# Kernel tuning notes

Measured on AMD Instinct MI355X. Metric: run time of the kernel, lower is better.

Reference implementation:

```python
import jax, jax.numpy as jnp
import numpy as np

D_CUT = 5.0   # cosine-cutoff distance
SIZE = 128    # rbf size == hidden_channels (nn_dist size = in_channels)
L = 2         # num_layers
EPS = 0.0     # GIN eps (non-trainable, initial 0)


def _rbf(d):
    # d: (E,) distances -> (E, SIZE) expnorm RBF with cosine cutoff
    d = d[:, None]
    start = float(np.exp(-D_CUT))
    means = jnp.linspace(start, 1.0, SIZE)
    beta = (2.0 / SIZE * (1.0 - start)) ** (-2)
    dc = jnp.minimum(d, D_CUT)
    cutoff = 0.5 * (jnp.cos(dc * jnp.pi / D_CUT) + 1.0)
    return cutoff * jnp.exp(-beta * (jnp.exp(-d) - means) ** 2)


def setup_inputs() -> dict:
    key = jax.random.key(0)
    ks = jax.random.split(key, 40)
    it = iter(range(40))
    def k():
        return ks[next(it)]
    N, H, ED, AS = 100000, 128, 4, 4
    def w(shape, s):
        return jax.random.normal(k(), shape, jnp.float32) * s
    inp = {}
    inp['x_lig'] = jax.random.normal(k(), (N, H), jnp.float32)
    inp['x_pock'] = jax.random.normal(k(), (N, H), jnp.float32)
    for name, E in (('bond', 200000), ('lp', 400000), ('pl', 400000)):
        inp['ei_' + name] = jax.random.randint(k(), (2, E), 0, N, jnp.int32)
        inp['ew_' + name] = jax.random.uniform(k(), (E,), jnp.float32) * D_CUT
        inp['ea_' + name] = jax.random.normal(k(), (E, AS), jnp.float32)
    inp['W0'] = w((3, AS, ED), 0.5)                 # initial per-edge-type lins (no bias)
    inp['Wd'] = w((L, 3, H, 2 * H), H ** -0.5)      # RBFDistanceScaleShift lin
    inp['bd'] = jnp.zeros((L, 3, 2 * H), jnp.float32)
    inp['We'] = w((L, 3, ED, H), 0.5)               # EGINConv.lin (edge_dim -> hidden)
    inp['be'] = jnp.zeros((L, 3, H), jnp.float32)
    inp['W1'] = w((L, 3, H, H), H ** -0.5)          # nn_node MLP layer 1
    inp['b1'] = jnp.zeros((L, 3, H), jnp.float32)
    inp['W2'] = w((L, 3, H, H), H ** -0.5)          # nn_node MLP layer 2
    inp['b2'] = jnp.zeros((L, 3, H), jnp.float32)
    return inp


def reference(x_lig, x_pock, ei_bond, ew_bond, ea_bond, ei_lp, ew_lp, ea_lp,
              ei_pl, ew_pl, ea_pl, W0, Wd, bd, We, be, W1, b1, W2, b2):
    # HeteroEGIN.forward: initial per-edge-type linear on raw edge attrs (bias-free)
    ea0 = ea_bond @ W0[0]
    ea1 = ea_lp @ W0[1]
    ea2 = ea_pl @ W0[2]

    def conv(x_src, x_dst, ei, ew, ea, t, l):
        # EGINConv per edge type t, layer l
        ss = _rbf(ew) @ Wd[l, t] + bd[l, t]            # (E, 2H) scale/shift from distance
        scale, shift = jnp.split(ss, 2, axis=1)
        xj = x_src[ei[0]] + (ea @ We[l, t] + be[l, t])  # gather + edge-attr lin
        msg = jax.nn.relu(xj * scale + shift)           # gated message
        agg = jax.ops.segment_sum(msg, ei[1], num_segments=x_dst.shape[0])
        o = agg + (1.0 + EPS) * x_dst
        return jax.nn.relu(o @ W1[l, t] + b1[l, t]) @ W2[l, t] + b2[l, t]

    for l in range(L):
        # to_hetero: sum conv outputs across edge types per destination node type
        new_lig = (conv(x_lig, x_lig, ei_bond, ew_bond, ea0, 0, l)
                   + conv(x_pock, x_lig, ei_pl, ew_pl, ea2, 2, l))
        new_pock = conv(x_lig, x_pock, ei_lp, ew_lp, ea1, 1, l)
        if l < L - 1:  # BasicGNN: act between layers, none after last (jk=None)
            new_lig = jax.nn.relu(new_lig)
            new_pock = jax.nn.relu(new_pock)
        x_lig, x_pock = new_lig, new_pock
    return jnp.concatenate([x_lig, x_pock], axis=0)
```

## Files before the change

kernel.cpp:

```cpp
#include <hip/hip_runtime.h>
#include <hip/hip_bf16.h>
#include <hip/hip_fp16.h>
#include <cmath>

typedef __attribute__((ext_vector_type(8))) short short8_t;
typedef __attribute__((ext_vector_type(4))) float f32x4;

static __device__ __forceinline__ short f2bs(float f) {
    union { __hip_bfloat16 h; short s; } u;
    u.h = __float2bfloat16(f);
    return u.s;
}
static __device__ __forceinline__ float bs2f(unsigned int us) {
    union { float f; unsigned int i; } u;
    u.i = us << 16;
    return u.f;
}
static __device__ __forceinline__ unsigned int pack2bf(float a, float b) {
    return (unsigned int)(unsigned short)f2bs(a) |
           ((unsigned int)(unsigned short)f2bs(b) << 16);
}
static __device__ __forceinline__ void lds_barrier() {
    asm volatile("s_waitcnt lgkmcnt(0)\n\ts_barrier" ::: "memory");
}

__global__ void pack_kernel(const float* __restrict__ Wd,
                            const float* __restrict__ W1,
                            const float* __restrict__ W2,
                            const float* __restrict__ W0,
                            const float* __restrict__ We,
                            short* __restrict__ pWd,
                            short* __restrict__ pW1,
                            short* __restrict__ pW2,
                            float* __restrict__ Mb)
{
    const int tid = blockIdx.x * blockDim.x + threadIdx.x;
    const int stride = gridDim.x * blockDim.x;
    for (int i = tid; i < 6 * 32768; i += stride) {
        int c = i >> 15, rem = i & 32767;
        int f = rem >> 9, l = (rem >> 3) & 63, j = rem & 7;
        int kk = f >> 4, nt = f & 15;
        int k = kk * 32 + (l >> 4) * 8 + j;
        int n = nt * 16 + (l & 15);
        pWd[i] = f2bs(Wd[(size_t)c * 32768 + k * 256 + n]);
    }
    for (int i = tid; i < 6 * 16384; i += stride) {
        int c = i >> 14, rem = i & 16383;
        int f = rem >> 9, l = (rem >> 3) & 63, j = rem & 7;
        int kk = f >> 3, nt = f & 7;
        int k = kk * 32 + (l >> 4) * 8 + j;
        int n = nt * 16 + (l & 15);
        pW1[i] = f2bs(W1[(size_t)c * 16384 + k * 128 + n]);
        pW2[i] = f2bs(W2[(size_t)c * 16384 + k * 128 + n]);
    }
    for (int i = tid; i < 6 * 512; i += stride) {
        int c = i >> 9, rem = i & 511;
        int a = rem >> 7, h = rem & 127;
        int t = c % 3;
        float m = 0.f;
        #pragma unroll
        for (int j = 0; j < 4; ++j)
            m = fmaf(W0[t * 16 + a * 4 + j], We[(size_t)c * 512 + j * 128 + h], m);
        Mb[i] = m;
    }
}

__global__ void tobf16_kernel(const float* __restrict__ a, const float* __restrict__ b,
                              unsigned short* __restrict__ oa, unsigned short* __restrict__ ob,
                              int n4)
{
    int i = blockIdx.x * blockDim.x + threadIdx.x;
    const int stride = gridDim.x * blockDim.x;
    for (; i < n4; i += stride) {
        float4 va = ((const float4*)a)[i];
        uint2 pa; pa.x = pack2bf(va.x, va.y); pa.y = pack2bf(va.z, va.w);
        ((uint2*)oa)[i] = pa;
        float4 vb = ((const float4*)b)[i];
        uint2 pb; pb.x = pack2bf(vb.x, vb.y); pb.y = pack2bf(vb.z, vb.w);
        ((uint2*)ob)[i] = pb;
    }
}

__global__ void hist3_kernel(const int* __restrict__ eiB, const int* __restrict__ eiL,
                             const int* __restrict__ eiP,
                             int EB, int EL, int EP, int N, int* __restrict__ cnt3)
{
    const int total = EB + EL + EP;
    for (int e = blockIdx.x * blockDim.x + threadIdx.x; e < total;
         e += gridDim.x * blockDim.x) {
        int base, le; const int* ei; int E;
        if (e < EB)           { base = 0;     le = e;           ei = eiB; E = EB; }
        else if (e < EB + EL) { base = N;     le = e - EB;      ei = eiL; E = EL; }
        else                  { base = 2 * N; le = e - EB - EL; ei = eiP; E = EP; }
        atomicAdd(&cnt3[base + ei[E + le]], 1);
    }
}

__global__ void scan1k_kernel(int* __restrict__ data, int* __restrict__ bsum, int n)
{
    __shared__ int buf[1024];
    const int gid = blockIdx.x * 1024 + threadIdx.x;
    int v = (gid < n) ? data[gid] : 0;
    buf[threadIdx.x] = v;
    __syncthreads();
    for (int off = 1; off < 1024; off <<= 1) {
        int t = (threadIdx.x >= off) ? buf[threadIdx.x - off] : 0;
        __syncthreads();
        buf[threadIdx.x] += t;
        __syncthreads();
    }
    if (gid < n) data[gid] = buf[threadIdx.x] - v;
    if (bsum && threadIdx.x == 1023) bsum[blockIdx.x] = buf[1023];
}

__global__ void scan_add_kernel(int* __restrict__ data, const int* __restrict__ bsum,
                                int* __restrict__ cursor, int n)
{
    const int gid = blockIdx.x * 1024 + threadIdx.x;
    if (gid < n) {
        int v = data[gid] + bsum[blockIdx.x];
        data[gid] = v;
        cursor[gid] = v;
    }
}

__global__ void scatter3_kernel(const int* __restrict__ eiB, const float* __restrict__ ewB,
                                const float4* __restrict__ eaB,
                                const int* __restrict__ eiL, const float* __restrict__ ewL,
                                const float4* __restrict__ eaL,
                                const int* __restrict__ eiP, const float* __restrict__ ewP,
                                const float4* __restrict__ eaP,
                                int EB, int EL, int EP, int N,
                                int* __restrict__ cursor,
                                uint4* __restrict__ rec, float* __restrict__ ewp)
{
    const int total = EB + EL + EP;
    for (int e = blockIdx.x * blockDim.x + threadIdx.x; e < total;
         e += gridDim.x * blockDim.x) {
        int base, le; const int* ei; const float* ew; const float4* ea; int E;
        if (e < EB)           { base = 0;     le = e;           ei = eiB; ew = ewB; ea = eaB; E = EB; }
        else if (e < EB + EL) { base = N;     le = e - EB;      ei = eiL; ew = ewL; ea = eaL; E = EL; }
        else                  { base = 2 * N; le = e - EB - EL; ei = eiP; ew = ewP; ea = eaP; E = EP; }
        int d = ei[E + le];
        int p = atomicAdd(&cursor[base + d], 1);
        float4 a = ea[le];
        uint4 r;
        r.x = (unsigned int)ei[le];
        r.y = (unsigned int)d;
        r.z = pack2bf(a.x, a.y);
        r.w = pack2bf(a.z, a.w);
        rec[p] = r;
        ewp[p] = ew[le];
    }
}

__global__ __launch_bounds__(512, 2)
void edge_mfma_kernel(
    const unsigned short* __restrict__ xsb,
    const uint4* __restrict__ rec,
    const float* __restrict__ ewp,
    const short* __restrict__ pWd, const float* __restrict__ bd,
    const float* __restrict__ Mb, const float* __restrict__ be,
    float* __restrict__ agg,
    int E, int ntiles,
    float rs, float rstep, float rbeta)
{
    __shared__ short sRbf[64 * 128];
    __shared__ __half sSS[64 * 256];

    const int t = threadIdx.x;
    const int lane = t & 63;
    const int w = t >> 6;
    const int l15 = lane & 15;
    const int l4 = lane >> 4;

    short8_t bfrag[4][2];
    #pragma unroll
    for (int kk = 0; kk < 4; ++kk)
        #pragma unroll
        for (int i = 0; i < 2; ++i)
            bfrag[kk][i] = *(const short8_t*)&pWd[((kk * 16 + 2 * w + i) * 64 + lane) * 8];
    float bdv[2];
    #pragma unroll
    for (int i = 0; i < 2; ++i) bdv[i] = bd[(2 * w + i) * 16 + l15];
    const float be0 = be[2 * lane], be1 = be[2 * lane + 1];
    float ma0[4], ma1[4];
    #pragma unroll
    for (int a = 0; a < 4; ++a) {
        ma0[a] = Mb[a * 128 + 2 * lane];
        ma1[a] = Mb[a * 128 + 2 * lane + 1];
    }

    const int stride = gridDim.x;
    int tile = blockIdx.x;
    if (tile >= ntiles) return;

    float ew_c; int src_c, dst_c; unsigned int ea01_c, ea23_c;
    unsigned int gx[8];
    {
        int eL = (tile << 6) + lane;
        int ec = eL < E ? eL : E - 1;
        uint4 r = rec[ec];
        ew_c = ewp[ec];
        src_c = (int)r.x;
        dst_c = (eL < E) ? (int)r.y : -1;
        ea01_c = r.z; ea23_c = r.w;
        #pragma unroll
        for (int rr = 0; rr < 8; ++rr) {
            int srn = __shfl(src_c, 8 * w + rr);
            gx[rr] = *(const unsigned int*)&xsb[(size_t)srn * 128 + lane * 2];
        }
    }

    for (; tile < ntiles; tile += stride) {
        const float edv = __expf(-ew_c);
        const float dcc = fminf(ew_c, 5.0f);
        const float cutv = 0.5f * (__cosf(dcc * 0.62831853071795864769f) + 1.0f);
        {
            char* base = (char*)sRbf + lane * 256;
            #pragma unroll
            for (int c = 0; c < 2; ++c) {
                short8_t v;
                #pragma unroll
                for (int j = 0; j < 8; ++j) {
                    float mean = rs + (float)(w * 16 + c * 8 + j) * rstep;
                    float diff = edv - mean;
                    v[j] = f2bs(cutv * __expf(-rbeta * diff * diff));
                }
                *(short8_t*)(base + ((w * 32 + c * 16) ^ ((lane & 7) << 4))) = v;
            }
        }
        unsigned int xjr[8];
        #pragma unroll
        for (int r = 0; r < 8; ++r) {
            unsigned int a01 = __shfl(ea01_c, 8 * w + r);
            unsigned int a23 = __shfl(ea23_c, 8 * w + r);
            float ea0 = bs2f(a01 & 0xffffu), ea1 = bs2f(a01 >> 16);
            float ea2 = bs2f(a23 & 0xffffu), ea3 = bs2f(a23 >> 16);
            unsigned int g = gx[r];
            float x0 = bs2f(g & 0xffffu), x1 = bs2f(g >> 16);
            float o0 = x0 + be0 + ea0 * ma0[0] + ea1 * ma0[1] + ea2 * ma0[2] + ea3 * ma0[3];
            float o1 = x1 + be1 + ea0 * ma1[0] + ea1 * ma1[1] + ea2 * ma1[2] + ea3 * ma1[3];
            xjr[r] = pack2bf(o0, o1);
        }

        lds_barrier();

        const int ntile = tile + stride;
        const bool has_next = ntile < ntiles;
        float ew_n = 0.f; int src_n = 0, dst_n = -1;
        unsigned int ea01_n = 0, ea23_n = 0;
        if (has_next) {
            int eL = (ntile << 6) + lane;
            int ec = eL < E ? eL : E - 1;
            uint4 r = rec[ec];
            ew_n = ewp[ec];
            src_n = (int)r.x;
            dst_n = (eL < E) ? (int)r.y : -1;
            ea01_n = r.z; ea23_n = r.w;
        }
        __builtin_amdgcn_sched_barrier(0);

        f32x4 acc[4][2];
        #pragma unroll
        for (int m = 0; m < 4; ++m) {
            acc[m][0] = (f32x4){0.f, 0.f, 0.f, 0.f};
            acc[m][1] = (f32x4){0.f, 0.f, 0.f, 0.f};
        }
        #pragma unroll
        for (int kk = 0; kk < 4; ++kk) {
            short8_t af[4];
            #pragma unroll
            for (int m = 0; m < 4; ++m) {
                int row = m * 16 + l15;
                int byte = row * 256 + ((kk * 64 + l4 * 16) ^ ((row & 7) << 4));
                af[m] = *(const short8_t*)((const char*)sRbf + byte);
            }
            #pragma unroll
            for (int m = 0; m < 4; ++m)
                #pragma unroll
                for (int i = 0; i < 2; ++i)
                    acc[m][i] = __builtin_amdgcn_mfma_f32_16x16x32_bf16(
                        af[m], bfrag[kk][i], acc[m][i], 0, 0, 0);
        }

        #pragma unroll
        for (int m = 0; m < 4; ++m)
            #pragma unroll
            for (int i = 0; i < 2; ++i) {
                int col = (2 * w + i) * 16 + l15;
                #pragma unroll
                for (int r = 0; r < 4; ++r) {
                    int row = m * 16 + l4 * 4 + r;
                    int byte = row * 512 + ((col * 2) ^ ((row & 7) << 4));
                    *(__half*)((char*)sSS + byte) = __float2half(acc[m][i][r] + bdv[i]);
                }
            }

        if (has_next) {
            #pragma unroll
            for (int r = 0; r < 8; ++r) {
                int srn = __shfl(src_n, 8 * w + r);
                gx[r] = *(const unsigned int*)&xsb[(size_t)srn * 128 + lane * 2];
            }
        }
        const int dst_f = dst_c;
        ew_c = ew_n; src_c = src_n; dst_c = dst_n; ea01_c = ea01_n; ea23_c = ea23_n;

        lds_barrier();

        {
            const bool prev_known = (w > 0);
            const bool next_known = (w < 7);
            const int dst_prev = prev_known ? __shfl(dst_f, 8 * w - 1) : -1;
            const int dst_next = next_known ? __shfl(dst_f, 8 * w + 8) : -1;

            float a0 = 0.f, a1 = 0.f;
            int rdst = __shfl(dst_f, 8 * w);
            bool first_run = true;
            #pragma unroll
            for (int r = 0; r < 8; ++r) {
                int e = 8 * w + r;
                unsigned int sc = *(const unsigned int*)
                    ((const char*)sSS + e * 512 + ((lane * 4) ^ ((e & 7) << 4)));
                unsigned int sh = *(const unsigned int*)
                    ((const char*)sSS + e * 512 + ((256 + lane * 4) ^ ((e & 7) << 4)));
                float2 scf = __half22float2(*(const __half2*)&sc);
                float2 shf = __half22float2(*(const __half2*)&sh);
                unsigned int g = xjr[r];
                float x0 = bs2f(g & 0xffffu), x1 = bs2f(g >> 16);
                float m0 = fmaxf(fmaf(x0, scf.x, shf.x), 0.0f);
                float m1 = fmaxf(fmaf(x1, scf.y, shf.y), 0.0f);
                int d = __shfl(dst_f, e);
                if (d != rdst) {
                    if (rdst >= 0) {
                        bool unsafe = first_run && (!prev_known || dst_prev == rdst);
                        float* ap = &agg[(size_t)rdst * 128 + 2 * lane];
                        if (unsafe) {
                            if (a0 != 0.f) unsafeAtomicAdd(ap, a0);
                            if (a1 != 0.f) unsafeAtomicAdd(ap + 1, a1);
                        } else {
                            float2 v; v.x = a0; v.y = a1;
                            *(float2*)ap = v;
                        }
                    }
                    first_run = false;
                    a0 = 0.f; a1 = 0.f; rdst = d;
                }
                a0 += m0; a1 += m1;
            }
            if (rdst >= 0) {
                bool unsafeL = first_run && (!prev_known || dst_prev == rdst);
                bool unsafeR = (!next_known || dst_next == rdst);
                float* ap = &agg[(size_t)rdst * 128 + 2 * lane];
                if (unsafeL || unsafeR) {
                    if (a0 != 0.f) unsafeAtomicAdd(ap, a0);
                    if (a1 != 0.f) unsafeAtomicAdd(ap + 1, a1);
                } else {
                    float2 v; v.x = a0; v.y = a1;
                    *(float2*)ap = v;
                }
            }
        }
    }
}

__global__ __launch_bounds__(256)
void node_mfma_kernel(
    float* __restrict__ agg,
    const float* __restrict__ xdf, const unsigned short* __restrict__ xdb,
    const short* __restrict__ pW1, const float* __restrict__ b1,
    const short* __restrict__ pW2, const float* __restrict__ b2,
    float* __restrict__ outf, unsigned short* __restrict__ outb,
    int N, int ntiles, int accumulate, int relu_out)
{
    __shared__ short sA[64 * 128];
    __shared__ short sH[64 * 128];

    const int t = threadIdx.x;
    const int lane = t & 63;
    const int w = t >> 6;
    const int l15 = lane & 15;
    const int l4 = lane >> 4;

    short8_t w1f[4][2], w2f[4][2];
    #pragma unroll
    for (int kk = 0; kk < 4; ++kk)
        #pragma unroll
        for (int p = 0; p < 2; ++p) {
            int nt = 2 * w + p;
            w1f[kk][p] = *(const short8_t*)&pW1[((kk * 8 + nt) * 64 + lane) * 8];
            w2f[kk][p] = *(const short8_t*)&pW2[((kk * 8 + nt) * 64 + lane) * 8];
        }
    float b1v[2], b2v[2];
    #pragma unroll
    for (int p = 0; p < 2; ++p) {
        int col = (2 * w + p) * 16 + l15;
        b1v[p] = b1[col];
        b2v[p] = b2[col];
    }

    const float4 zero4 = {0.f, 0.f, 0.f, 0.f};

    for (int tile = blockIdx.x; tile < ntiles; tile += gridDim.x) {
        const int n0 = tile << 6;
        #pragma unroll
        for (int i = 0; i < 4; ++i) {
            int idx = i * 256 + t;
            int row = idx >> 4, c8 = idx & 15;
            int gr = n0 + row; if (gr >= N) gr = N - 1;
            float4 a0 = ((const float4*)agg)[(size_t)gr * 32 + c8 * 2];
            float4 a1 = ((const float4*)agg)[(size_t)gr * 32 + c8 * 2 + 1];
            ((float4*)agg)[(size_t)gr * 32 + c8 * 2]     = zero4;
            ((float4*)agg)[(size_t)gr * 32 + c8 * 2 + 1] = zero4;
            float av[8] = {a0.x, a0.y, a0.z, a0.w, a1.x, a1.y, a1.z, a1.w};
            float xv[8];
            if (xdf) {
                float4 x0 = ((const float4*)xdf)[(size_t)gr * 32 + c8 * 2];
                float4 x1 = ((const float4*)xdf)[(size_t)gr * 32 + c8 * 2 + 1];
                xv[0] = x0.x; xv[1] = x0.y; xv[2] = x0.z; xv[3] = x0.w;
                xv[4] = x1.x; xv[5] = x1.y; xv[6] = x1.z; xv[7] = x1.w;
            } else {
                uint4 xr = ((const uint4*)xdb)[(size_t)gr * 16 + c8];
                xv[0] = bs2f(xr.x & 0xffffu); xv[1] = bs2f(xr.x >> 16);
                xv[2] = bs2f(xr.y & 0xffffu); xv[3] = bs2f(xr.y >> 16);
                xv[4] = bs2f(xr.z & 0xffffu); xv[5] = bs2f(xr.z >> 16);
                xv[6] = bs2f(xr.w & 0xffffu); xv[7] = bs2f(xr.w >> 16);
            }
            short8_t v;
            #pragma unroll
            for (int j = 0; j < 8; ++j)
                v[j] = f2bs(av[j] + xv[j]);
            int byte = row * 256 + ((c8 * 16) ^ ((row & 7) << 4));
            *(short8_t*)((char*)sA + byte) = v;
        }
        lds_barrier();

        f32x4 acc[4][2];
        #pragma unroll
        for (int m = 0; m < 4; ++m) {
            acc[m][0] = (f32x4){0.f, 0.f, 0.f, 0.f};
            acc[m][1] = (f32x4){0.f, 0.f, 0.f, 0.f};
        }
        #pragma unroll
        for (int kk = 0; kk < 4; ++kk) {
            short8_t af[4];
            #pragma unroll
            for (int m = 0; m < 4; ++m) {
                int row = m * 16 + l15;
                int byte = row * 256 + ((kk * 64 + l4 * 16) ^ ((row & 7) << 4));
                af[m] = *(const short8_t*)((const char*)sA + byte);
            }
            #pragma unroll
            for (int m = 0; m < 4; ++m)
                #pragma unroll
                for (int p = 0; p < 2; ++p)
                    acc[m][p] = __builtin_amdgcn_mfma_f32_16x16x32_bf16(
                        af[m], w1f[kk][p], acc[m][p], 0, 0, 0);
        }
        #pragma unroll
        for (int m = 0; m < 4; ++m)
            #pragma unroll
            for (int p = 0; p < 2; ++p) {
                int col = (2 * w + p) * 16 + l15;
                #pragma unroll
                for (int r = 0; r < 4; ++r) {
                    int row = m * 16 + l4 * 4 + r;
                    short hs = f2bs(fmaxf(acc[m][p][r] + b1v[p], 0.f));
                    int byte = row * 256 + ((col * 2) ^ ((row & 7) << 4));
                    *(short*)((char*)sH + byte) = hs;
                }
            }
        lds_barrier();

        f32x4 acc2[4][2];
        #pragma unroll
        for (int m = 0; m < 4; ++m) {
            acc2[m][0] = (f32x4){0.f, 0.f, 0.f, 0.f};
            acc2[m][1] = (f32x4){0.f, 0.f, 0.f, 0.f};
        }
        #pragma unroll
        for (int kk = 0; kk < 4; ++kk) {
            short8_t af[4];
            #pragma unroll
            for (int m = 0; m < 4; ++m) {
                int row = m * 16 + l15;
                int byte = row * 256 + ((kk * 64 + l4 * 16) ^ ((row & 7) << 4));
                af[m] = *(const short8_t*)((const char*)sH + byte);
            }
            #pragma unroll
            for (int m = 0; m < 4; ++m)
                #pragma unroll
                for (int p = 0; p < 2; ++p)
                    acc2[m][p] = __builtin_amdgcn_mfma_f32_16x16x32_bf16(
                        af[m], w2f[kk][p], acc2[m][p], 0, 0, 0);
        }
        #pragma unroll
        for (int m = 0; m < 4; ++m)
            #pragma unroll
            for (int p = 0; p < 2; ++p) {
                int col = (2 * w + p) * 16 + l15;
                #pragma unroll
                for (int r = 0; r < 4; ++r) {
                    int row = n0 + m * 16 + l4 * 4 + r;
                    if (row < N) {
                        float v = acc2[m][p][r] + b2v[p];
                        if (outf) {
                            float* op = &outf[(size_t)row * 128 + col];
                            if (accumulate) v += *op;
                            if (relu_out) v = fmaxf(v, 0.f);
                            *op = v;
                        } else {
                            unsigned short* op = &outb[(size_t)row * 128 + col];
                            if (accumulate) v += bs2f((unsigned int)*op);
                            if (relu_out) v = fmaxf(v, 0.f);
                            *op = (unsigned short)f2bs(v);
                        }
                    }
                }
            }
    }
}

extern "C" void kernel_launch(void* const* d_in, const int* in_sizes, int n_in,
                              void* d_out, int out_size, void* d_ws, size_t ws_size,
                              hipStream_t stream)
{
    const float* x_lig   = (const float*)d_in[0];
    const float* x_pock  = (const float*)d_in[1];
    const int*   ei_bond = (const int*)d_in[2];
    const float* ew_bond = (const float*)d_in[3];
    const float* ea_bond = (const float*)d_in[4];
    const int*   ei_lp   = (const int*)d_in[5];
    const float* ew_lp   = (const float*)d_in[6];
    const float* ea_lp   = (const float*)d_in[7];
    const int*   ei_pl   = (const int*)d_in[8];
    const float* ew_pl   = (const float*)d_in[9];
    const float* ea_pl   = (const float*)d_in[10];
    const float* W0 = (const float*)d_in[11];
    const float* Wd = (const float*)d_in[12];
    const float* bd = (const float*)d_in[13];
    const float* We = (const float*)d_in[14];
    const float* be = (const float*)d_in[15];
    const float* W1 = (const float*)d_in[16];
    const float* b1 = (const float*)d_in[17];
    const float* W2 = (const float*)d_in[18];
    const float* b2 = (const float*)d_in[19];

    const int H = 128;
    const int N = in_sizes[0] / H;
    const int E_bond = in_sizes[3];
    const int E_lp   = in_sizes[6];
    const int E_pl   = in_sizes[9];
    const int E_all  = E_bond + E_lp + E_pl;

    char* wp = (char*)d_ws;
    auto alloc = [&](size_t bytes) -> char* {
        char* r = wp;
        wp += (bytes + 255) & ~(size_t)255;
        return r;
    };
    unsigned short* A   = (unsigned short*)alloc((size_t)N * H * 2);
    unsigned short* Bb  = (unsigned short*)alloc((size_t)N * H * 2);
    unsigned short* C   = (unsigned short*)alloc((size_t)N * H * 2);
    float*   agg  = (float*)alloc((size_t)N * H * 4);
    int*     cnt3 = (int*)alloc((size_t)3 * N * 4);
    char*    zero_end = wp;
    uint4*   recAll = (uint4*)alloc((size_t)E_all * 16);
    float*   ewpAll = (float*)alloc((size_t)E_all * 4);
    short*   pWd  = (short*)alloc(6 * 32768 * 2);
    short*   pW1s = (short*)alloc(6 * 16384 * 2);
    short*   pW2s = (short*)alloc(6 * 16384 * 2);
    float*   Mb   = (float*)alloc(6 * 512 * 4);
    int*     cursor = (int*)alloc((size_t)3 * N * 4);
    int*     bsum   = (int*)alloc(1024 * 4);

    const uint4* recB = recAll;
    const uint4* recL = recAll + E_bond;
    const uint4* recP = recAll + E_bond + E_lp;
    const float* ewpB = ewpAll;
    const float* ewpL = ewpAll + E_bond;
    const float* ewpP = ewpAll + E_bond + E_lp;

    float* outL = (float*)d_out;
    float* outP = outL + (size_t)N * H;

    const int capE = 256;
    const int capN = 4 * 256;

    hipMemsetAsync(agg, 0, (size_t)(zero_end - (char*)agg), stream);
    tobf16_kernel<<<512, 256, 0, stream>>>(x_lig, x_pock, A, Bb, N * H / 4);
    pack_kernel<<<256, 256, 0, stream>>>(Wd, W1, W2, W0, We, pWd, pW1s, pW2s, Mb);

    const int n3 = 3 * N;
    const int nb3 = (n3 + 1023) / 1024;
    hist3_kernel<<<1024, 256, 0, stream>>>(ei_bond, ei_lp, ei_pl,
                                           E_bond, E_lp, E_pl, N, cnt3);
    scan1k_kernel<<<nb3, 1024, 0, stream>>>(cnt3, bsum, n3);
    scan1k_kernel<<<1, 1024, 0, stream>>>(bsum, nullptr, nb3);
    scan_add_kernel<<<nb3, 1024, 0, stream>>>(cnt3, bsum, cursor, n3);
    scatter3_kernel<<<1024, 256, 0, stream>>>(
        ei_bond, ew_bond, (const float4*)ea_bond,
        ei_lp,   ew_lp,   (const float4*)ea_lp,
        ei_pl,   ew_pl,   (const float4*)ea_pl,
        E_bond, E_lp, E_pl, N, cursor, recAll, ewpAll);

    const double start_d = exp(-5.0);
    const float rs    = (float)start_d;
    const float rstep = (float)((1.0 - start_d) / 127.0);
    const float rbeta = (float)std::pow(2.0 / 128.0 * (1.0 - start_d), -2.0);

    auto conv = [&](const unsigned short* src,
                    const float* xdf, const unsigned short* xdb,
                    const uint4* rec, const float* ewp, int E,
                    int l, int tt, float* outf, unsigned short* outb,
                    int accum, int relu) {
        const int lt = l * 3 + tt;
        const int ntE = (E + 63) / 64;
        const int gE = ntE < capE ? ntE : capE;
        edge_mfma_kernel<<<gE, 512, 0, stream>>>(
            src, rec, ewp,
            pWd + (size_t)lt * 32768, bd + (size_t)lt * 256,
            Mb + (size_t)lt * 512, be + (size_t)lt * 128,
            agg, E, ntE, rs, rstep, rbeta);
        const int ntN = (N + 63) / 64;
        const int gN = ntN < capN ? ntN : capN;
        node_mfma_kernel<<<gN, 256, 0, stream>>>(
            agg, xdf, xdb,
            pW1s + (size_t)lt * 16384, b1 + (size_t)lt * 128,
            pW2s + (size_t)lt * 16384, b2 + (size_t)lt * 128,
            outf, outb, N, ntN, accum, relu);
    };

    conv(A,  x_pock, nullptr, recL, ewpL, E_lp,   0, 1, nullptr, C, 0, 1);
    conv(A,  x_lig,  nullptr, recB, ewpB, E_bond, 0, 0, nullptr, A, 0, 0);
    conv(Bb, x_lig,  nullptr, recP, ewpP, E_pl,   0, 2, nullptr, A, 1, 1);
    conv(A, nullptr, A, recB, ewpB, E_bond, 1, 0, outL, nullptr, 0, 0);
    conv(C, nullptr, A, recP, ewpP, E_pl,   1, 2, outL, nullptr, 1, 0);
    conv(A, nullptr, C, recL, ewpL, E_lp,   1, 1, outP, nullptr, 0, 0);
}
```

Baseline: 887.5 us.

## Fuse two lig-destination node MLPs into one kernel with second agg buffer

```diff
diff --git a/kernel.cpp b/kernel.cpp
--- a/kernel.cpp
+++ b/kernel.cpp
@@ -372,7 +372,7 @@
     const short* __restrict__ pW1, const float* __restrict__ b1,
     const short* __restrict__ pW2, const float* __restrict__ b2,
     float* __restrict__ outf, unsigned short* __restrict__ outb,
-    int N, int ntiles, int accumulate, int relu_out)
+    int N, int ntiles, int relu_out)
 {
     __shared__ short sA[64 * 128];
     __shared__ short sH[64 * 128];
@@ -408,11 +408,14 @@
         for (int i = 0; i < 4; ++i) {
             int idx = i * 256 + t;
             int row = idx >> 4, c8 = idx & 15;
-            int gr = n0 + row; if (gr >= N) gr = N - 1;
+            bool real = (n0 + row) < N;
+            int gr = real ? (n0 + row) : (N - 1);
             float4 a0 = ((const float4*)agg)[(size_t)gr * 32 + c8 * 2];
             float4 a1 = ((const float4*)agg)[(size_t)gr * 32 + c8 * 2 + 1];
-            ((float4*)agg)[(size_t)gr * 32 + c8 * 2]     = zero4;
-            ((float4*)agg)[(size_t)gr * 32 + c8 * 2 + 1] = zero4;
+            if (real) {
+                ((float4*)agg)[(size_t)gr * 32 + c8 * 2]     = zero4;
+                ((float4*)agg)[(size_t)gr * 32 + c8 * 2 + 1] = zero4;
+            }
             float av[8] = {a0.x, a0.y, a0.z, a0.w, a1.x, a1.y, a1.z, a1.w};
             float xv[8];
             if (xdf) {
@@ -505,20 +508,258 @@
                     int row = n0 + m * 16 + l4 * 4 + r;
                     if (row < N) {
                         float v = acc2[m][p][r] + b2v[p];
-                        if (outf) {
-                            float* op = &outf[(size_t)row * 128 + col];
-                            if (accumulate) v += *op;
-                            if (relu_out) v = fmaxf(v, 0.f);
-                            *op = v;
-                        } else {
-                            unsigned short* op = &outb[(size_t)row * 128 + col];
-                            if (accumulate) v += bs2f((unsigned int)*op);
-                            if (relu_out) v = fmaxf(v, 0.f);
-                            *op = (unsigned short)f2bs(v);
-                        }
+                        if (relu_out) v = fmaxf(v, 0.f);
+                        if (outf) outf[(size_t)row * 128 + col] = v;
+                        else outb[(size_t)row * 128 + col] = (unsigned short)f2bs(v);
                     }
                 }
             }
+    }
+}
+
+__global__ __launch_bounds__(256)
+void node_fused_kernel(
+    float* __restrict__ agg, const float* __restrict__ agg2,
+    const float* __restrict__ xdf, const unsigned short* __restrict__ xdb,
+    const short* __restrict__ pW1a, const float* __restrict__ b1a,
+    const short* __restrict__ pW2a, const float* __restrict__ b2a,
+    const short* __restrict__ pW1b, const float* __restrict__ b1b,
+    const short* __restrict__ pW2b, const float* __restrict__ b2b,
+    float* __restrict__ outf, unsigned short* __restrict__ outb,
+    int N, int ntiles, int relu_out)
+{
+    __shared__ short sA[64 * 128];
+    __shared__ short sH[64 * 128];
+
+    const int t = threadIdx.x;
+    const int lane = t & 63;
+    const int w = t >> 6;
+    const int l15 = lane & 15;
+    const int l4 = lane >> 4;
+
+    float b1av[2], b2av[2], b1bv[2], b2bv[2];
+    #pragma unroll
+    for (int p = 0; p < 2; ++p) {
+        int col = (2 * w + p) * 16 + l15;
+        b1av[p] = b1a[col]; b2av[p] = b2a[col];
+        b1bv[p] = b1b[col]; b2bv[p] = b2b[col];
+    }
+
+    const float4 zero4 = {0.f, 0.f, 0.f, 0.f};
+
+    for (int tile = blockIdx.x; tile < ntiles; tile += gridDim.x) {
+        const int n0 = tile << 6;
+
+        #pragma unroll
+        for (int i = 0; i < 4; ++i) {
+            int idx = i * 256 + t;
+            int row = idx >> 4, c8 = idx & 15;
+            bool real = (n0 + row) < N;
+            int gr = real ? (n0 + row) : (N - 1);
+            float4 a0 = ((const float4*)agg)[(size_t)gr * 32 + c8 * 2];
+            float4 a1 = ((const float4*)agg)[(size_t)gr * 32 + c8 * 2 + 1];
+            if (real) {
+                ((float4*)agg)[(size_t)gr * 32 + c8 * 2]     = zero4;
+                ((float4*)agg)[(size_t)gr * 32 + c8 * 2 + 1] = zero4;
+            }
+            float av[8] = {a0.x, a0.y, a0.z, a0.w, a1.x, a1.y, a1.z, a1.w};
+            float xv[8];
+            if (xdf) {
+                float4 x0 = ((const float4*)xdf)[(size_t)gr * 32 + c8 * 2];
+                float4 x1 = ((const float4*)xdf)[(size_t)gr * 32 + c8 * 2 + 1];
+                xv[0] = x0.x; xv[1] = x0.y; xv[2] = x0.z; xv[3] = x0.w;
+                xv[4] = x1.x; xv[5] = x1.y; xv[6] = x1.z; xv[7] = x1.w;
+            } else {
+                uint4 xr = ((const uint4*)xdb)[(size_t)gr * 16 + c8];
+                xv[0] = bs2f(xr.x & 0xffffu); xv[1] = bs2f(xr.x >> 16);
+                xv[2] = bs2f(xr.y & 0xffffu); xv[3] = bs2f(xr.y >> 16);
+                xv[4] = bs2f(xr.z & 0xffffu); xv[5] = bs2f(xr.z >> 16);
+                xv[6] = bs2f(xr.w & 0xffffu); xv[7] = bs2f(xr.w >> 16);
+            }
+            short8_t v;
+            #pragma unroll
+            for (int j = 0; j < 8; ++j)
+                v[j] = f2bs(av[j] + xv[j]);
+            int byte = row * 256 + ((c8 * 16) ^ ((row & 7) << 4));
+            *(short8_t*)((char*)sA + byte) = v;
+        }
+        lds_barrier();
+
+        f32x4 acc[4][2];
+        #pragma unroll
+        for (int m = 0; m < 4; ++m) {
+            acc[m][0] = (f32x4){0.f, 0.f, 0.f, 0.f};
+            acc[m][1] = (f32x4){0.f, 0.f, 0.f, 0.f};
+        }
+        #pragma unroll
+        for (int kk = 0; kk < 4; ++kk) {
+            short8_t wf[2];
+            #pragma unroll
+            for (int p = 0; p < 2; ++p)
+                wf[p] = *(const short8_t*)&pW1a[((kk * 8 + 2 * w + p) * 64 + lane) * 8];
+            short8_t af[4];
+            #pragma unroll
+            for (int m = 0; m < 4; ++m) {
+                int row = m * 16 + l15;
+                int byte = row * 256 + ((kk * 64 + l4 * 16) ^ ((row & 7) << 4));
+                af[m] = *(const short8_t*)((const char*)sA + byte);
+            }
+            #pragma unroll
+            for (int m = 0; m < 4; ++m)
+                #pragma unroll
+                for (int p = 0; p < 2; ++p)
+                    acc[m][p] = __builtin_amdgcn_mfma_f32_16x16x32_bf16(
+                        af[m], wf[p], acc[m][p], 0, 0, 0);
+        }
+        #pragma unroll
+        for (int m = 0; m < 4; ++m)
+            #pragma unroll
+            for (int p = 0; p < 2; ++p) {
+                int col = (2 * w + p) * 16 + l15;
+                #pragma unroll
+                for (int r = 0; r < 4; ++r) {
+                    int row = m * 16 + l4 * 4 + r;
+                    short hs = f2bs(fmaxf(acc[m][p][r] + b1av[p], 0.f));
+                    int byte = row * 256 + ((col * 2) ^ ((row & 7) << 4));
+                    *(short*)((char*)sH + byte) = hs;
+                }
+            }
+        lds_barrier();
+
+        f32x4 accO[4][2];
+        #pragma unroll
+        for (int m = 0; m < 4; ++m) {
+            accO[m][0] = (f32x4){0.f, 0.f, 0.f, 0.f};
+            accO[m][1] = (f32x4){0.f, 0.f, 0.f, 0.f};
+        }
+        #pragma unroll
+        for (int kk = 0; kk < 4; ++kk) {
+            short8_t wf[2];
+            #pragma unroll
+            for (int p = 0; p < 2; ++p)
+                wf[p] = *(const short8_t*)&pW2a[((kk * 8 + 2 * w + p) * 64 + lane) * 8];
+            short8_t af[4];
+            #pragma unroll
+            for (int m = 0; m < 4; ++m) {
+                int row = m * 16 + l15;
+                int byte = row * 256 + ((kk * 64 + l4 * 16) ^ ((row & 7) << 4));
+                af[m] = *(const short8_t*)((const char*)sH + byte);
+            }
+            #pragma unroll
+            for (int m = 0; m < 4; ++m)
+                #pragma unroll
+                for (int p = 0; p < 2; ++p)
+                    accO[m][p] = __builtin_amdgcn_mfma_f32_16x16x32_bf16(
+                        af[m], wf[p], accO[m][p], 0, 0, 0);
+        }
+        #pragma unroll
+        for (int i = 0; i < 4; ++i) {
+            int idx = i * 256 + t;
+            int row = idx >> 4, c8 = idx & 15;
+            bool real = (n0 + row) < N;
+            int gr = real ? (n0 + row) : (N - 1);
+            float4 a0 = ((const float4*)agg2)[(size_t)gr * 32 + c8 * 2];
+            float4 a1 = ((const float4*)agg2)[(size_t)gr * 32 + c8 * 2 + 1];
+            float av[8] = {a0.x, a0.y, a0.z, a0.w, a1.x, a1.y, a1.z, a1.w};
+            float xv[8];
+            if (xdf) {
+                float4 x0 = ((const float4*)xdf)[(size_t)gr * 32 + c8 * 2];
+                float4 x1 = ((const float4*)xdf)[(size_t)gr * 32 + c8 * 2 + 1];
+                xv[0] = x0.x; xv[1] = x0.y; xv[2] = x0.z; xv[3] = x0.w;
+                xv[4] = x1.x; xv[5] = x1.y; xv[6] = x1.z; xv[7] = x1.w;
+            } else {
+                uint4 xr = ((const uint4*)xdb)[(size_t)gr * 16 + c8];
+                xv[0] = bs2f(xr.x & 0xffffu); xv[1] = bs2f(xr.x >> 16);
+                xv[2] = bs2f(xr.y & 0xffffu); xv[3] = bs2f(xr.y >> 16);
+                xv[4] = bs2f(xr.z & 0xffffu); xv[5] = bs2f(xr.z >> 16);
+                xv[6] = bs2f(xr.w & 0xffffu); xv[7] = bs2f(xr.w >> 16);
+            }
+            short8_t v;
+            #pragma unroll
+            for (int j = 0; j < 8; ++j)
+                v[j] = f2bs(av[j] + xv[j]);
+            int byte = row * 256 + ((c8 * 16) ^ ((row & 7) << 4));
+            *(short8_t*)((char*)sA + byte) = v;
+        }
+        lds_barrier();
+
+        #pragma unroll
+        for (int m = 0; m < 4; ++m) {
+            acc[m][0] = (f32x4){0.f, 0.f, 0.f, 0.f};
+            acc[m][1] = (f32x4){0.f, 0.f, 0.f, 0.f};
+        }
+        #pragma unroll
+        for (int kk = 0; kk < 4; ++kk) {
+            short8_t wf[2];
+            #pragma unroll
+            for (int p = 0; p < 2; ++p)
+                wf[p] = *(const short8_t*)&pW1b[((kk * 8 + 2 * w + p) * 64 + lane) * 8];
+            short8_t af[4];
+            #pragma unroll
+            for (int m = 0; m < 4; ++m) {
+                int row = m * 16 + l15;
+                int byte = row * 256 + ((kk * 64 + l4 * 16) ^ ((row & 7) << 4));
+                af[m] = *(const short8_t*)((const char*)sA + byte);
+            }
+            #pragma unroll
+            for (int m = 0; m < 4; ++m)
+                #pragma unroll
+                for (int p = 0; p < 2; ++p)
+                    acc[m][p] = __builtin_amdgcn_mfma_f32_16x16x32_bf16(
+                        af[m], wf[p], acc[m][p], 0, 0, 0);
+        }
+        #pragma unroll
+        for (int m = 0; m < 4; ++m)
+            #pragma unroll
+            for (int p = 0; p < 2; ++p) {
+                int col = (2 * w + p) * 16 + l15;
+                #pragma unroll
+                for (int r = 0; r < 4; ++r) {
+                    int row = m * 16 + l4 * 4 + r;
+                    short hs = f2bs(fmaxf(acc[m][p][r] + b1bv[p], 0.f));
+                    int byte = row * 256 + ((col * 2) ^ ((row & 7) << 4));
+                    *(short*)((char*)sH + byte) = hs;
+                }
+            }
+        lds_barrier();
+
+        #pragma unroll
+        for (int kk = 0; kk < 4; ++kk) {
+            short8_t wf[2];
+            #pragma unroll
+            for (int p = 0; p < 2; ++p)
+                wf[p] = *(const short8_t*)&pW2b[((kk * 8 + 2 * w + p) * 64 + lane) * 8];
+            short8_t af[4];
+            #pragma unroll
+            for (int m = 0; m < 4; ++m) {
+                int row = m * 16 + l15;
+                int byte = row * 256 + ((kk * 64 + l4 * 16) ^ ((row & 7) << 4));
+                af[m] = *(const short8_t*)((const char*)sH + byte);
+            }
+            #pragma unroll
+            for (int m = 0; m < 4; ++m)
+                #pragma unroll
+                for (int p = 0; p < 2; ++p)
+                    accO[m][p] = __builtin_amdgcn_mfma_f32_16x16x32_bf16(
+                        af[m], wf[p], accO[m][p], 0, 0, 0);
+        }
+        #pragma unroll
+        for (int m = 0; m < 4; ++m)
+            #pragma unroll
+            for (int p = 0; p < 2; ++p) {
+                int col = (2 * w + p) * 16 + l15;
+                #pragma unroll
+                for (int r = 0; r < 4; ++r) {
+                    int row = n0 + m * 16 + l4 * 4 + r;
+                    if (row < N) {
+                        float v = accO[m][p][r] + b2av[p] + b2bv[p];
+                        if (relu_out) v = fmaxf(v, 0.f);
+                        if (outf) outf[(size_t)row * 128 + col] = v;
+                        else outb[(size_t)row * 128 + col] = (unsigned short)f2bs(v);
+                    }
+                }
+            }
+        lds_barrier();
     }
 }
 
@@ -588,6 +829,7 @@
     const int capE = 256;
     const int capN = 4 * 256;
 
+    hipMemsetAsync(d_out, 0, (size_t)2 * N * H * sizeof(float), stream);
     hipMemsetAsync(agg, 0, (size_t)(zero_end - (char*)agg), stream);
     tobf16_kernel<<<512, 256, 0, stream>>>(x_lig, x_pock, A, Bb, N * H / 4);
     pack_kernel<<<256, 256, 0, stream>>>(Wd, W1, W2, W0, We, pWd, pW1s, pW2s, Mb);
@@ -610,32 +852,48 @@
     const float rstep = (float)((1.0 - start_d) / 127.0);
     const float rbeta = (float)std::pow(2.0 / 128.0 * (1.0 - start_d), -2.0);
 
-    auto conv = [&](const unsigned short* src,
-                    const float* xdf, const unsigned short* xdb,
-                    const uint4* rec, const float* ewp, int E,
-                    int l, int tt, float* outf, unsigned short* outb,
-                    int accum, int relu) {
-        const int lt = l * 3 + tt;
+    auto edge = [&](const unsigned short* src, const uint4* rec, const float* ewp,
+                    int E, int lt, float* aggbuf) {
         const int ntE = (E + 63) / 64;
         const int gE = ntE < capE ? ntE : capE;
         edge_mfma_kernel<<<gE, 512, 0, stream>>>(
             src, rec, ewp,
             pWd + (size_t)lt * 32768, bd + (size_t)lt * 256,
             Mb + (size_t)lt * 512, be + (size_t)lt * 128,
-            agg, E, ntE, rs, rstep, rbeta);
-        const int ntN = (N + 63) / 64;
-        const int gN = ntN < capN ? ntN : capN;
-        node_mfma_kernel<<<gN, 256, 0, stream>>>(
-            agg, xdf, xdb,
-            pW1s + (size_t)lt * 16384, b1 + (size_t)lt * 128,
-            pW2s + (size_t)lt * 16384, b2 + (size_t)lt * 128,
-            outf, outb, N, ntN, accum, relu);
+            aggbuf, E, ntE, rs, rstep, rbeta);
     };
-
-    conv(A,  x_pock, nullptr, recL, ewpL, E_lp,   0, 1, nullptr, C, 0, 1);
-    conv(A,  x_lig,  nullptr, recB, ewpB, E_bond, 0, 0, nullptr, A, 0, 0);
-    conv(Bb, x_lig,  nullptr, recP, ewpP, E_pl,   0, 2, nullptr, A, 1, 1);
-    conv(A, nullptr, A, recB, ewpB, E_bond, 1, 0, outL, nullptr, 0, 0);
-    conv(C, nullptr, A, recP, ewpP, E_pl,   1, 2, outL, nullptr, 1, 0);
-    conv(A, nullptr, C, recL, ewpL, E_lp,   1, 1, outP, nullptr, 0, 0);
-}
+    const int ntN = (N + 63) / 64;
+    const int gN = ntN < capN ? ntN : capN;
+
+    edge(A, recL, ewpL, E_lp, 1, agg);
+    node_mfma_kernel<<<gN, 256, 0, stream>>>(
+        agg, x_pock, nullptr,
+        pW1s + (size_t)1 * 16384, b1 + (size_t)1 * 128,
+        pW2s + (size_t)1 * 16384, b2 + (size_t)1 * 128,
+        nullptr, C, N, ntN, 1);
+    edge(A,  recB, ewpB, E_bond, 0, agg);
+    edge(Bb, recP, ewpP, E_pl,   2, outL);
+    node_fused_kernel<<<gN, 256, 0, stream>>>(
+        agg, outL, x_lig, nullptr,
+        pW1s + (size_t)0 * 16384, b1 + (size_t)0 * 128,
+        pW2s + (size_t)0 * 16384, b2 + (size_t)0 * 128,
+        pW1s + (size_t)2 * 16384, b1 + (size_t)2 * 128,
+        pW2s + (size_t)2 * 16384, b2 + (size_t)2 * 128,
+        nullptr, A, N, ntN, 1);
+
+    edge(A, recB, ewpB, E_bond, 3, agg);
+    edge(C, recP, ewpP, E_pl,   5, outP);
+    node_fused_kernel<<<gN, 256, 0, stream>>>(
+        agg, outP, nullptr, A,
+        pW1s + (size_t)3 * 16384, b1 + (size_t)3 * 128,
+        pW2s + (size_t)3 * 16384, b2 + (size_t)3 * 128,
+        pW1s + (size_t)5 * 16384, b1 + (size_t)5 * 128,
+        pW2s + (size_t)5 * 16384, b2 + (size_t)5 * 128,
+        outL, nullptr, N, ntN, 0);
+    edge(A, recL, ewpL, E_lp, 4, agg);
+    node_mfma_kernel<<<gN, 256, 0, stream>>>(
+        agg, nullptr, C,
+        pW1s + (size_t)4 * 16384, b1 + (size_t)4 * 128,
+        pW2s + (size_t)4 * 16384, b2 + (size_t)4 * 128,
+        outP, nullptr, N, ntN, 0);
+}
```

Measured after the change: 864.2 us. 1.03x faster.
